# Optimization experiments

Measured on AMD Instinct MI355X. Metric: run time of the kernel, lower is better.

Reference implementation:

```python
import jax, jax.numpy as jnp
import numpy as np


def _dwconv(x, w, pad):
    # depthwise conv, NCHW, weight (C,1,kh,kw), feature_group_count=C
    return jax.lax.conv_general_dilated(
        x, w, window_strides=(1, 1), padding=pad,
        feature_group_count=x.shape[1],
        dimension_numbers=('NCHW', 'OIHW', 'NCHW'))


def _max_channel_relu(x):
    # assumed MaxChannelReLU: keep only the channel-max value at each (b,h,w)
    return x * (x == jnp.max(x, axis=1, keepdims=True))


def setup_inputs() -> dict:
    key = jax.random.key(0)
    ks = jax.random.split(key, 6)
    B, C, H, W = 16, 64, 128, 128
    x = jax.random.normal(ks[0], (B, C, H, W), dtype=jnp.float32)
    w_bbx = 0.1 * jax.random.normal(ks[1], (C, 1, 1, 1), dtype=jnp.float32)
    w_width = 0.1 * jax.random.normal(ks[2], (C, 1, 1, 11), dtype=jnp.float32)
    w_width_sh = 0.1 * jax.random.normal(ks[3], (C, 1, 1, 1), dtype=jnp.float32)
    w_height = 0.1 * jax.random.normal(ks[4], (C, 1, 11, 1), dtype=jnp.float32)
    w_height_sh = 0.1 * jax.random.normal(ks[5], (C, 1, 1, 1), dtype=jnp.float32)
    return {"x": x, "w_bbx": w_bbx, "w_width": w_width,
            "w_width_sh": w_width_sh, "w_height": w_height,
            "w_height_sh": w_height_sh}


def reference(x, w_bbx, w_width, w_width_sh, w_height, w_height_sh):
    B, C, H, W = x.shape
    # self.bbx: depthwise 1x1 conv == per-channel scale
    wh = x * w_bbx.reshape(1, C, 1, 1)
    # width branch: depthwise (1,11) conv pad 5, scaled by W, then shared 1x1
    w = _dwconv(wh, w_width, [(0, 0), (5, 5)]) * W
    w = w * w_width_sh.reshape(1, C, 1, 1)
    # height branch: depthwise (11,1) conv pad 5, scaled by H, then shared 1x1
    h = _dwconv(wh, w_height, [(5, 5), (0, 0)]) * H
    h = h * w_height_sh.reshape(1, C, 1, 1)
    sx = jax.nn.sigmoid(x)
    M = jnp.max(sx, axis=(-2, -1), keepdims=True) - 0.01
    score = x * (sx > M).astype(x.dtype)
    S = jnp.sum(score, axis=(-2, -1), keepdims=True)
    sn = score / S  # normalized weights, reused by all weighted reductions
    ws = jnp.sum(w * sn, axis=(-2, -1))
    hs = jnp.sum(h * sn, axis=(-2, -1))
    ps = jnp.max(sx, axis=(-2, -1))
    col = jnp.arange(W, dtype=x.dtype).reshape(1, 1, 1, W)
    row = jnp.arange(H, dtype=x.dtype).reshape(1, 1, H, 1)
    x1 = jnp.sum(col * sn, axis=(-2, -1)) - ws / 2
    y1 = jnp.sum(row * sn, axis=(-2, -1)) - hs / 2
    x2 = x1 + ws
    y2 = y1 + hs
    score_m = _max_channel_relu(score)
    w_m = _max_channel_relu(w)
    h_m = _max_channel_relu(h)
    i = jnp.broadcast_to(jnp.arange(B, dtype=x.dtype)[:, None], (B, C))
    bbox = jnp.stack([i, x1, y1, x2, y2, ps], axis=-1).reshape(-1, 6)
    return jnp.concatenate([score_m, w_m, h_m], axis=1), bbox
```

## Files before the change

### kernel.cpp

```cpp
#include <hip/hip_runtime.h>
#include <math.h>

#define BATCH 16
#define CH    64
#define HH    128
#define WW    128
#define PLANE (HH*WW)
#define LROW  144
#define HROWS 74
#define OUT0  (BATCH*3*CH*PLANE)


__global__ __launch_bounds__(256) void k_max(const float* __restrict__ x,
                                             float* __restrict__ ws) {
    int bid = blockIdx.x;
    const float4* xp = (const float4*)(x + (size_t)bid * PLANE);
    int tid = threadIdx.x;
    float m = -INFINITY;
#pragma unroll
    for (int i = 0; i < 16; i++) {
        float4 v = xp[i * 256 + tid];
        m = fmaxf(m, fmaxf(fmaxf(v.x, v.y), fmaxf(v.z, v.w)));
    }
#pragma unroll
    for (int off = 32; off; off >>= 1) m = fmaxf(m, __shfl_xor(m, off, 64));
    __shared__ float sm[4];
    int wid = tid >> 6, lane = tid & 63;
    if (lane == 0) sm[wid] = m;
    __syncthreads();
    if (tid == 0) {
        float mm = fmaxf(fmaxf(sm[0], sm[1]), fmaxf(sm[2], sm[3]));
        float ps = 1.0f / (1.0f + expf(-mm));
        ws[bid] = ps - 0.01f;
        ws[1024 + bid] = ps;
        ws[2048 + bid] = 0.0f;
        ws[3072 + bid] = 0.0f;
        ws[4096 + bid] = 0.0f;
        ws[5120 + bid] = 0.0f;
        ws[6144 + bid] = 0.0f;
    }
}

__global__ __launch_bounds__(256) void k_fields(
    const float* __restrict__ x,
    const float* __restrict__ w_bbx, const float* __restrict__ w_width,
    const float* __restrict__ w_width_sh, const float* __restrict__ w_height,
    const float* __restrict__ w_height_sh,
    float* __restrict__ ws, float* __restrict__ out) {
    __shared__ float4 xs4[HROWS * (LROW / 4)];
    __shared__ float red[4 * 5];
    float* xs = (float*)xs4;
    int bid2 = blockIdx.x;
    int bc = bid2 >> 1, half = bid2 & 1;
    int r0 = half * 64;
    int b = bc >> 6, c = bc & 63;
    int tid = threadIdx.x;

    for (int j = tid; j < HROWS * (LROW / 4); j += 256)
        xs4[j] = make_float4(0.f, 0.f, 0.f, 0.f);
    __syncthreads();
    const float* xp = x + (size_t)bc * PLANE;
    for (int j = tid; j < HROWS * 32; j += 256) {
        int i = j >> 5, c4 = j & 31;
        int gr = r0 - 5 + i;
        if ((unsigned)gr < 128u)
            *(float4*)&xs[i * LROW + 8 + c4 * 4] = ((const float4*)xp)[gr * 32 + c4];
    }
    float wk[11], hk[11];
#pragma unroll
    for (int k = 0; k < 11; k++) {
        wk[k] = w_width[c * 11 + k];
        hk[k] = w_height[c * 11 + k];
    }
    float cb = w_bbx[c];
    float cw = 128.0f * w_width_sh[c] * cb;
    float chs = 128.0f * w_height_sh[c] * cb;
    float M = ws[bc];
    __syncthreads();

    float S = 0.f, Sw = 0.f, Sh = 0.f, Scol = 0.f, Srow = 0.f;
    float* outS = out + (size_t)(b * 192 + c) * PLANE;
    float* outW = out + (size_t)(b * 192 + 64 + c) * PLANE;
    float* outH = out + (size_t)(b * 192 + 128 + c) * PLANE;
    int obase = r0 * 32;

    for (int g = 0; g < 8; g++) {
        int idx = g * 256 + tid;
        int p = idx * 4;
        int y = p >> 7, xc = p & 127;
        float4 vx;
        float hx = 0.f, hy = 0.f, hz = 0.f, hw = 0.f;
#pragma unroll
        for (int k = 0; k < 11; k++) {
            float4 v = *(const float4*)&xs[(y + k) * LROW + xc + 8];
            if (k == 5) vx = v;
            hx += v.x * hk[k]; hy += v.y * hk[k];
            hz += v.z * hk[k]; hw += v.w * hk[k];
        }
        float wbuf[20];
        {
            float4 a0 = *(const float4*)&xs[(y + 5) * LROW + xc + 0];
            float4 a1 = *(const float4*)&xs[(y + 5) * LROW + xc + 4];
            float4 a3 = *(const float4*)&xs[(y + 5) * LROW + xc + 12];
            float4 a4 = *(const float4*)&xs[(y + 5) * LROW + xc + 16];
            wbuf[0] = a0.x;  wbuf[1] = a0.y;  wbuf[2] = a0.z;  wbuf[3] = a0.w;
            wbuf[4] = a1.x;  wbuf[5] = a1.y;  wbuf[6] = a1.z;  wbuf[7] = a1.w;
            wbuf[8] = vx.x;  wbuf[9] = vx.y;  wbuf[10] = vx.z; wbuf[11] = vx.w;
            wbuf[12] = a3.x; wbuf[13] = a3.y; wbuf[14] = a3.z; wbuf[15] = a3.w;
            wbuf[16] = a4.x; wbuf[17] = a4.y; wbuf[18] = a4.z; wbuf[19] = a4.w;
        }
        float wo[4];
#pragma unroll
        for (int j = 0; j < 4; j++) {
            float acc = 0.f;
#pragma unroll
            for (int k = 0; k < 11; k++) acc += wbuf[j + 3 + k] * wk[k];
            wo[j] = acc * cw;
        }
        float ho[4] = {hx * chs, hy * chs, hz * chs, hw * chs};
        float xv[4] = {vx.x, vx.y, vx.z, vx.w};
        float sc[4];
#pragma unroll
        for (int j = 0; j < 4; j++) {
            float sx = 1.0f / (1.0f + expf(-xv[j]));
            sc[j] = (sx > M) ? xv[j] : 0.0f;
        }
        float s4 = sc[0] + sc[1] + sc[2] + sc[3];
        S += s4;
        Srow += (float)(r0 + y) * s4;
#pragma unroll
        for (int j = 0; j < 4; j++) {
            Sw += wo[j] * sc[j];
            Sh += ho[j] * sc[j];
            Scol += (float)(xc + j) * sc[j];
        }
        float4 o;
        o.x = sc[0]; o.y = sc[1]; o.z = sc[2]; o.w = sc[3];
        ((float4*)outS)[obase + idx] = o;
        o.x = wo[0]; o.y = wo[1]; o.z = wo[2]; o.w = wo[3];
        ((float4*)outW)[obase + idx] = o;
        o.x = ho[0]; o.y = ho[1]; o.z = ho[2]; o.w = ho[3];
        ((float4*)outH)[obase + idx] = o;
    }
#pragma unroll
    for (int off = 32; off; off >>= 1) {
        S    += __shfl_xor(S, off, 64);
        Sw   += __shfl_xor(Sw, off, 64);
        Sh   += __shfl_xor(Sh, off, 64);
        Scol += __shfl_xor(Scol, off, 64);
        Srow += __shfl_xor(Srow, off, 64);
    }
    int wid = tid >> 6, lane = tid & 63;
    if (lane == 0) {
        red[wid * 5 + 0] = S;   red[wid * 5 + 1] = Sw;
        red[wid * 5 + 2] = Sh;  red[wid * 5 + 3] = Scol;
        red[wid * 5 + 4] = Srow;
    }
    __syncthreads();
    if (tid == 0) {
        float a0 = 0, a1 = 0, a2 = 0, a3 = 0, a4 = 0;
#pragma unroll
        for (int w2 = 0; w2 < 4; w2++) {
            a0 += red[w2 * 5 + 0]; a1 += red[w2 * 5 + 1];
            a2 += red[w2 * 5 + 2]; a3 += red[w2 * 5 + 3];
            a4 += red[w2 * 5 + 4];
        }
        atomicAdd(&ws[2048 + bc], a0);
        atomicAdd(&ws[3072 + bc], a1);
        atomicAdd(&ws[4096 + bc], a2);
        atomicAdd(&ws[5120 + bc], a3);
        atomicAdd(&ws[6144 + bc], a4);
    }
}

__global__ __launch_bounds__(256) void k_mask(float* __restrict__ out) {
    int chunk = blockIdx.x;
    int f = blockIdx.y;
    int b = blockIdx.z;
    int tid = threadIdx.x;
    size_t base = ((size_t)b * 192 + (size_t)f * 64) * PLANE
                + (size_t)chunk * 256 + tid;
    float v[64];
#pragma unroll
    for (int c = 0; c < 64; c++) v[c] = out[base + (size_t)c * PLANE];
    float m = v[0];
#pragma unroll
    for (int c = 1; c < 64; c++) m = fmaxf(m, v[c]);
#pragma unroll
    for (int c = 0; c < 64; c++)
        out[base + (size_t)c * PLANE] = (v[c] == m) ? v[c] : 0.0f;
}

__global__ __launch_bounds__(256) void k_bbox(const float* __restrict__ ws,
                                              float* __restrict__ out) {
    int idx = blockIdx.x * 256 + threadIdx.x;
    if (idx >= 1024) return;
    int b = idx >> 6;
    float S    = ws[2048 + idx];
    float Sw   = ws[3072 + idx];
    float Sh   = ws[4096 + idx];
    float Scol = ws[5120 + idx];
    float Srow = ws[6144 + idx];
    float ps   = ws[1024 + idx];
    float inv = 1.0f / S;
    float wsv = Sw * inv, hsv = Sh * inv;
    float x1 = Scol * inv - 0.5f * wsv;
    float y1 = Srow * inv - 0.5f * hsv;
    float* o = out + OUT0 + (size_t)idx * 6;
    o[0] = (float)b;
    o[1] = x1;
    o[2] = y1;
    o[3] = x1 + wsv;
    o[4] = y1 + hsv;
    o[5] = ps;
}

extern "C" void kernel_launch(void* const* d_in, const int* in_sizes, int n_in,
                              void* d_out, int out_size, void* d_ws, size_t ws_size,
                              hipStream_t stream) {
    const float* x          = (const float*)d_in[0];
    const float* w_bbx      = (const float*)d_in[1];
    const float* w_width    = (const float*)d_in[2];
    const float* w_width_sh = (const float*)d_in[3];
    const float* w_height   = (const float*)d_in[4];
    const float* w_height_sh= (const float*)d_in[5];
    float* out = (float*)d_out;
    float* ws  = (float*)d_ws;

    k_max<<<dim3(1024), dim3(256), 0, stream>>>(x, ws);
    k_fields<<<dim3(2048), dim3(256), 0, stream>>>(
        x, w_bbx, w_width, w_width_sh, w_height, w_height_sh, ws, out);
    k_mask<<<dim3(64, 3, 16), dim3(256), 0, stream>>>(out);
    k_bbox<<<dim3(4), dim3(256), 0, stream>>>(ws, out);
}
```

Measured before the change: 317.9 us.

## Replace write-then-mask passes with channel-argmax keys and one scatter write

```diff
diff --git a/kernel.cpp b/kernel.cpp
--- a/kernel.cpp
+++ b/kernel.cpp
@@ -7,24 +7,53 @@
 #define WW    128
 #define PLANE (HH*WW)
 #define LROW  144
-#define HROWS 74
+#define LROWS 138
 #define OUT0  (BATCH*3*CH*PLANE)
-
-
-__global__ __launch_bounds__(256) void k_max(const float* __restrict__ x,
-                                             float* __restrict__ ws) {
+#define SR4   36
+#define SROWS 26
+#define MBOFF 8192
+#define MBN   786432
+
+
+__device__ __forceinline__ unsigned enc32(float f) {
+    unsigned u = __float_as_uint(f);
+    return (u & 0x80000000u) ? ~u : (u | 0x80000000u);
+}
+__device__ __forceinline__ float dec32(unsigned k) {
+    unsigned u = (k & 0x80000000u) ? (k ^ 0x80000000u) : ~k;
+    return __uint_as_float(u);
+}
+
+__global__ __launch_bounds__(256) void k_stats(
+    const float* __restrict__ x,
+    const float* __restrict__ w_bbx, const float* __restrict__ w_width,
+    const float* __restrict__ w_width_sh, const float* __restrict__ w_height,
+    const float* __restrict__ w_height_sh,
+    float* __restrict__ ws) {
+    __shared__ float xs[LROWS * LROW];
+    __shared__ float red[4 * 5];
+    __shared__ float sm[5];
     int bid = blockIdx.x;
-    const float4* xp = (const float4*)(x + (size_t)bid * PLANE);
+    int b = bid >> 6, c = bid & 63;
+    (void)b;
     int tid = threadIdx.x;
+
+    for (int j = tid; j < LROWS * LROW / 4; j += 256)
+        ((float4*)xs)[j] = make_float4(0.f, 0.f, 0.f, 0.f);
+    __syncthreads();
+    const float* xp = x + (size_t)bid * PLANE;
     float m = -INFINITY;
 #pragma unroll
     for (int i = 0; i < 16; i++) {
-        float4 v = xp[i * 256 + tid];
+        int idx = i * 256 + tid;
+        int p = idx * 4;
+        int y = p >> 7, xc = p & 127;
+        float4 v = ((const float4*)xp)[idx];
         m = fmaxf(m, fmaxf(fmaxf(v.x, v.y), fmaxf(v.z, v.w)));
+        *(float4*)&xs[(y + 5) * LROW + xc + 8] = v;
     }
 #pragma unroll
     for (int off = 32; off; off >>= 1) m = fmaxf(m, __shfl_xor(m, off, 64));
-    __shared__ float sm[4];
     int wid = tid >> 6, lane = tid & 63;
     if (lane == 0) sm[wid] = m;
     __syncthreads();
@@ -33,38 +62,7 @@
         float ps = 1.0f / (1.0f + expf(-mm));
         ws[bid] = ps - 0.01f;
         ws[1024 + bid] = ps;
-        ws[2048 + bid] = 0.0f;
-        ws[3072 + bid] = 0.0f;
-        ws[4096 + bid] = 0.0f;
-        ws[5120 + bid] = 0.0f;
-        ws[6144 + bid] = 0.0f;
-    }
-}
-
-__global__ __launch_bounds__(256) void k_fields(
-    const float* __restrict__ x,
-    const float* __restrict__ w_bbx, const float* __restrict__ w_width,
-    const float* __restrict__ w_width_sh, const float* __restrict__ w_height,
-    const float* __restrict__ w_height_sh,
-    float* __restrict__ ws, float* __restrict__ out) {
-    __shared__ float4 xs4[HROWS * (LROW / 4)];
-    __shared__ float red[4 * 5];
-    float* xs = (float*)xs4;
-    int bid2 = blockIdx.x;
-    int bc = bid2 >> 1, half = bid2 & 1;
-    int r0 = half * 64;
-    int b = bc >> 6, c = bc & 63;
-    int tid = threadIdx.x;
-
-    for (int j = tid; j < HROWS * (LROW / 4); j += 256)
-        xs4[j] = make_float4(0.f, 0.f, 0.f, 0.f);
-    __syncthreads();
-    const float* xp = x + (size_t)bc * PLANE;
-    for (int j = tid; j < HROWS * 32; j += 256) {
-        int i = j >> 5, c4 = j & 31;
-        int gr = r0 - 5 + i;
-        if ((unsigned)gr < 128u)
-            *(float4*)&xs[i * LROW + 8 + c4 * 4] = ((const float4*)xp)[gr * 32 + c4];
+        sm[4] = ps - 0.01f;
     }
     float wk[11], hk[11];
 #pragma unroll
@@ -75,16 +73,11 @@
     float cb = w_bbx[c];
     float cw = 128.0f * w_width_sh[c] * cb;
     float chs = 128.0f * w_height_sh[c] * cb;
-    float M = ws[bc];
     __syncthreads();
+    float M = sm[4];
 
     float S = 0.f, Sw = 0.f, Sh = 0.f, Scol = 0.f, Srow = 0.f;
-    float* outS = out + (size_t)(b * 192 + c) * PLANE;
-    float* outW = out + (size_t)(b * 192 + 64 + c) * PLANE;
-    float* outH = out + (size_t)(b * 192 + 128 + c) * PLANE;
-    int obase = r0 * 32;
-
-    for (int g = 0; g < 8; g++) {
+    for (int g = 0; g < 16; g++) {
         int idx = g * 256 + tid;
         int p = idx * 4;
         int y = p >> 7, xc = p & 127;
@@ -127,20 +120,13 @@
         }
         float s4 = sc[0] + sc[1] + sc[2] + sc[3];
         S += s4;
-        Srow += (float)(r0 + y) * s4;
+        Srow += (float)y * s4;
 #pragma unroll
         for (int j = 0; j < 4; j++) {
             Sw += wo[j] * sc[j];
             Sh += ho[j] * sc[j];
             Scol += (float)(xc + j) * sc[j];
         }
-        float4 o;
-        o.x = sc[0]; o.y = sc[1]; o.z = sc[2]; o.w = sc[3];
-        ((float4*)outS)[obase + idx] = o;
-        o.x = wo[0]; o.y = wo[1]; o.z = wo[2]; o.w = wo[3];
-        ((float4*)outW)[obase + idx] = o;
-        o.x = ho[0]; o.y = ho[1]; o.z = ho[2]; o.w = ho[3];
-        ((float4*)outH)[obase + idx] = o;
     }
 #pragma unroll
     for (int off = 32; off; off >>= 1) {
@@ -150,7 +136,6 @@
         Scol += __shfl_xor(Scol, off, 64);
         Srow += __shfl_xor(Srow, off, 64);
     }
-    int wid = tid >> 6, lane = tid & 63;
     if (lane == 0) {
         red[wid * 5 + 0] = S;   red[wid * 5 + 1] = Sw;
         red[wid * 5 + 2] = Sh;  red[wid * 5 + 3] = Scol;
@@ -165,30 +150,166 @@
             a2 += red[w2 * 5 + 2]; a3 += red[w2 * 5 + 3];
             a4 += red[w2 * 5 + 4];
         }
-        atomicAdd(&ws[2048 + bc], a0);
-        atomicAdd(&ws[3072 + bc], a1);
-        atomicAdd(&ws[4096 + bc], a2);
-        atomicAdd(&ws[5120 + bc], a3);
-        atomicAdd(&ws[6144 + bc], a4);
-    }
-}
-
-__global__ __launch_bounds__(256) void k_mask(float* __restrict__ out) {
+        ws[2048 + bid] = a0;
+        ws[3072 + bid] = a1;
+        ws[4096 + bid] = a2;
+        ws[5120 + bid] = a3;
+        ws[6144 + bid] = a4;
+    }
+}
+
+__global__ __launch_bounds__(512) void k_maxch(
+    const float* __restrict__ x,
+    const float* __restrict__ w_bbx, const float* __restrict__ w_width,
+    const float* __restrict__ w_width_sh, const float* __restrict__ w_height,
+    const float* __restrict__ w_height_sh,
+    const float* __restrict__ ws, unsigned long long* __restrict__ mb) {
+    __shared__ float4 xs4[2][SROWS * SR4];
+    int t = blockIdx.x;
+    int half = blockIdx.y;
+    int b = blockIdx.z;
+    int tid = threadIdx.x;
+    int r = tid >> 5, q = tid & 31;
+
+    for (int j = tid; j < 2 * SROWS * SR4; j += 512)
+        ((float4*)xs4)[j] = make_float4(0.f, 0.f, 0.f, 0.f);
+
+    int cbase = half * 32;
+    {
+        const float* xp = x + (size_t)(b * 64 + cbase) * PLANE;
+        for (int j = tid; j < SROWS * 32; j += 512) {
+            int i = j >> 5, c4 = j & 31;
+            int gr = t * 16 - 5 + i;
+            float4 v = make_float4(0.f, 0.f, 0.f, 0.f);
+            if ((unsigned)gr < 128u) v = ((const float4*)xp)[gr * 32 + c4];
+            xs4[0][i * SR4 + 2 + c4] = v;
+        }
+    }
+    unsigned long long kW[4], kH[4], kS[4];
+#pragma unroll
+    for (int j = 0; j < 4; j++) { kW[j] = 0ull; kH[j] = 0ull; kS[j] = 0ull; }
+
+    int cur = 0;
+    for (int cc = 0; cc < 32; cc++) {
+        __syncthreads();
+        int c = cbase + cc;
+        float4 p0 = make_float4(0.f, 0.f, 0.f, 0.f);
+        float4 p1 = make_float4(0.f, 0.f, 0.f, 0.f);
+        bool have = (cc + 1 < 32);
+        if (have) {
+            const float* xp = x + (size_t)(b * 64 + c + 1) * PLANE;
+            int i0 = tid >> 5, c40 = tid & 31;
+            int gr0 = t * 16 - 5 + i0;
+            if ((unsigned)gr0 < 128u) p0 = ((const float4*)xp)[gr0 * 32 + c40];
+            if (tid < 320) {
+                int gr1 = gr0 + 16;
+                if ((unsigned)gr1 < 128u) p1 = ((const float4*)xp)[gr1 * 32 + c40];
+            }
+        }
+        float wkc[11], hkc[11];
+#pragma unroll
+        for (int k = 0; k < 11; k++) {
+            wkc[k] = w_width[c * 11 + k];
+            hkc[k] = w_height[c * 11 + k];
+        }
+        float cb = w_bbx[c];
+        float cw = 128.0f * w_width_sh[c] * cb;
+        float chs = 128.0f * w_height_sh[c] * cb;
+        float M = ws[b * 64 + c];
+
+        float4 vx;
+        float hx = 0.f, hy = 0.f, hz = 0.f, hw = 0.f;
+#pragma unroll
+        for (int k = 0; k < 11; k++) {
+            float4 v = xs4[cur][(r + k) * SR4 + 2 + q];
+            if (k == 5) vx = v;
+            hx += v.x * hkc[k]; hy += v.y * hkc[k];
+            hz += v.z * hkc[k]; hw += v.w * hkc[k];
+        }
+        float wbuf[20];
+        {
+            float4 a0 = xs4[cur][(r + 5) * SR4 + q + 0];
+            float4 a1 = xs4[cur][(r + 5) * SR4 + q + 1];
+            float4 a3 = xs4[cur][(r + 5) * SR4 + q + 3];
+            float4 a4 = xs4[cur][(r + 5) * SR4 + q + 4];
+            wbuf[0] = a0.x;  wbuf[1] = a0.y;  wbuf[2] = a0.z;  wbuf[3] = a0.w;
+            wbuf[4] = a1.x;  wbuf[5] = a1.y;  wbuf[6] = a1.z;  wbuf[7] = a1.w;
+            wbuf[8] = vx.x;  wbuf[9] = vx.y;  wbuf[10] = vx.z; wbuf[11] = vx.w;
+            wbuf[12] = a3.x; wbuf[13] = a3.y; wbuf[14] = a3.z; wbuf[15] = a3.w;
+            wbuf[16] = a4.x; wbuf[17] = a4.y; wbuf[18] = a4.z; wbuf[19] = a4.w;
+        }
+        float wo[4];
+#pragma unroll
+        for (int j = 0; j < 4; j++) {
+            float acc = 0.f;
+#pragma unroll
+            for (int k = 0; k < 11; k++) acc += wbuf[j + 3 + k] * wkc[k];
+            wo[j] = acc * cw;
+        }
+        float ho[4] = {hx * chs, hy * chs, hz * chs, hw * chs};
+        float xv[4] = {vx.x, vx.y, vx.z, vx.w};
+#pragma unroll
+        for (int j = 0; j < 4; j++) {
+            float sx = 1.0f / (1.0f + expf(-xv[j]));
+            float sc = (sx > M) ? xv[j] : 0.0f;
+            unsigned long long cand;
+            cand = ((unsigned long long)enc32(sc) << 32) | (unsigned)c;
+            if (cand > kS[j]) kS[j] = cand;
+            cand = ((unsigned long long)enc32(wo[j]) << 32) | (unsigned)c;
+            if (cand > kW[j]) kW[j] = cand;
+            cand = ((unsigned long long)enc32(ho[j]) << 32) | (unsigned)c;
+            if (cand > kH[j]) kH[j] = cand;
+        }
+        if (have) {
+            xs4[cur ^ 1][(tid >> 5) * SR4 + 2 + (tid & 31)] = p0;
+            if (tid < 320)
+                xs4[cur ^ 1][((tid >> 5) + 16) * SR4 + 2 + (tid & 31)] = p1;
+        }
+        cur ^= 1;
+    }
+    int gr = t * 16 + r;
+    size_t pix = (size_t)gr * 128 + 4 * q;
+    unsigned long long* o = mb + (size_t)half * MBN;
+    size_t i0 = (size_t)(b * 3 + 0) * 16384 + pix;
+    size_t i1 = (size_t)(b * 3 + 1) * 16384 + pix;
+    size_t i2 = (size_t)(b * 3 + 2) * 16384 + pix;
+#pragma unroll
+    for (int j = 0; j < 4; j++) {
+        o[i0 + j] = kS[j];
+        o[i1 + j] = kW[j];
+        o[i2 + j] = kH[j];
+    }
+}
+
+__global__ __launch_bounds__(256) void k_scatter(
+    const unsigned long long* __restrict__ mb, float* __restrict__ out) {
     int chunk = blockIdx.x;
     int f = blockIdx.y;
     int b = blockIdx.z;
     int tid = threadIdx.x;
-    size_t base = ((size_t)b * 192 + (size_t)f * 64) * PLANE
-                + (size_t)chunk * 256 + tid;
-    float v[64];
-#pragma unroll
-    for (int c = 0; c < 64; c++) v[c] = out[base + (size_t)c * PLANE];
-    float m = v[0];
-#pragma unroll
-    for (int c = 1; c < 64; c++) m = fmaxf(m, v[c]);
-#pragma unroll
-    for (int c = 0; c < 64; c++)
-        out[base + (size_t)c * PLANE] = (v[c] == m) ? v[c] : 0.0f;
+    size_t pix = (size_t)chunk * 1024 + tid * 4;
+    size_t ki = (size_t)(b * 3 + f) * 16384 + pix;
+    const unsigned long long* m0 = mb;
+    const unsigned long long* m1 = mb + MBN;
+    float val[4];
+    int win[4];
+#pragma unroll
+    for (int j = 0; j < 4; j++) {
+        unsigned long long k0 = m0[ki + j], k1 = m1[ki + j];
+        unsigned long long k = (k0 > k1) ? k0 : k1;
+        val[j] = dec32((unsigned)(k >> 32));
+        win[j] = (int)(k & 63u);
+    }
+    float* ob = out + (size_t)(b * 192 + f * 64) * PLANE + pix;
+#pragma unroll
+    for (int c = 0; c < 64; c++) {
+        float4 o;
+        o.x = (win[0] == c) ? val[0] : 0.f;
+        o.y = (win[1] == c) ? val[1] : 0.f;
+        o.z = (win[2] == c) ? val[2] : 0.f;
+        o.w = (win[3] == c) ? val[3] : 0.f;
+        *(float4*)&ob[(size_t)c * PLANE] = o;
+    }
 }
 
 __global__ __launch_bounds__(256) void k_bbox(const float* __restrict__ ws,
@@ -226,10 +347,12 @@
     const float* w_height_sh= (const float*)d_in[5];
     float* out = (float*)d_out;
     float* ws  = (float*)d_ws;
-
-    k_max<<<dim3(1024), dim3(256), 0, stream>>>(x, ws);
-    k_fields<<<dim3(2048), dim3(256), 0, stream>>>(
-        x, w_bbx, w_width, w_width_sh, w_height, w_height_sh, ws, out);
-    k_mask<<<dim3(64, 3, 16), dim3(256), 0, stream>>>(out);
+    unsigned long long* mb = (unsigned long long*)(ws + MBOFF);
+
+    k_stats<<<dim3(1024), dim3(256), 0, stream>>>(
+        x, w_bbx, w_width, w_width_sh, w_height, w_height_sh, ws);
+    k_maxch<<<dim3(8, 2, 16), dim3(512), 0, stream>>>(
+        x, w_bbx, w_width, w_width_sh, w_height, w_height_sh, ws, mb);
+    k_scatter<<<dim3(16, 3, 16), dim3(256), 0, stream>>>(mb, out);
     k_bbox<<<dim3(4), dim3(256), 0, stream>>>(ws, out);
 }
```

Result: slower. 362.0 us (+13.9%).
